# Kernel tuning notes

Measured on AMD Instinct MI355X. Metric: run time of the kernel, lower is better.

The kernel has to match this reference:

```python
import jax, jax.numpy as jnp
import numpy as np

NUM_CLASSES = 10000
EMBED_DIM = 128
BATCH = 4096
SCALE = 10.0
FOCAL_ALPHA = 0.25
FOCAL_GAMMA = 2.0
HARD_NEG_RATIO = 0.3


def setup_inputs() -> dict:
    key = jax.random.key(0)
    k1, k2, k3, k4 = jax.random.split(key, 4)
    embeddings = jax.random.normal(k1, (BATCH, EMBED_DIM), dtype=jnp.float32)
    labels = jax.random.randint(k2, (BATCH,), 0, NUM_CLASSES)
    class_weights = jax.random.uniform(k3, (NUM_CLASSES,), dtype=jnp.float32)
    # kaiming_normal_(mode='fan_out') on [C, D] -> std = sqrt(2 / C)
    proxies = jax.random.normal(k4, (NUM_CLASSES, EMBED_DIM), dtype=jnp.float32) * np.sqrt(2.0 / NUM_CLASSES)
    return {"embeddings": embeddings, "labels": labels,
            "class_weights": class_weights, "proxies": proxies}


def reference(embeddings, labels, class_weights, proxies):
    C = proxies.shape[0]
    # L2 normalize (F.normalize with eps=1e-12)
    e = embeddings / jnp.maximum(jnp.linalg.norm(embeddings, axis=1, keepdims=True), 1e-12)
    p = proxies / jnp.maximum(jnp.linalg.norm(proxies, axis=1, keepdims=True), 1e-12)
    sim = jnp.einsum('bd,cd->bc', e, p) * SCALE  # [B, C]

    pos_sim = jnp.take_along_axis(sim, labels[:, None], axis=1)[:, 0]  # [B]

    # mask out the positive class, then top-k hard negatives (k is static)
    k = max(1, int((C - 1) * HARD_NEG_RATIO))
    is_pos = labels[:, None] == jnp.arange(C)[None, :]
    neg_sim = jnp.where(is_pos, -jnp.inf, sim)
    hard_neg, _ = jax.lax.top_k(neg_sim, k)  # [B, k]

    combined = jnp.concatenate([pos_sim[:, None], hard_neg], axis=1)  # [B, 1+k]
    probs = jax.nn.softmax(combined, axis=1)
    pos_prob = probs[:, 0]

    ce = -jnp.log(pos_prob + 1e-8)
    focal = FOCAL_ALPHA * (1.0 - pos_prob) ** FOCAL_GAMMA * ce
    weighted = focal * class_weights[labels]
    return jnp.sum(weighted) / embeddings.shape[0]
```

## Files before the change

kernel.cpp:

```cpp
#include <hip/hip_runtime.h>
#include <hip/hip_bf16.h>
#include <hip/hip_fp16.h>


#define BATCH   4096
#define NCLASS  10000
#define EDIM    128
#define KSEL    2999
#define LDK     136
#define MLOG    10.0f

typedef __attribute__((ext_vector_type(8))) short short8;
typedef __attribute__((ext_vector_type(4))) float floatx4;

__device__ __forceinline__ unsigned short f2bf(float f) {
    unsigned int u = __float_as_uint(f);
    unsigned int r = (u + 0x7FFFu + ((u >> 16) & 1u)) >> 16;
    return (unsigned short)r;
}
__device__ __forceinline__ unsigned int f2key16(float x) {
    unsigned short hb = __half_as_ushort(__float2half(x));
    return (hb & 0x8000u) ? (unsigned int)(~hb & 0xFFFFu)
                          : (unsigned int)(hb | 0x8000u);
}
__device__ __forceinline__ float key16val(unsigned int k) {
    unsigned short hb = (k & 0x8000u) ? (unsigned short)(k ^ 0x8000u)
                                      : (unsigned short)(~k & 0xFFFFu);
    return __half2float(__ushort_as_half(hb));
}

__global__ __launch_bounds__(256) void prep_kernel(
    const float* __restrict__ emb, const float* __restrict__ px,
    unsigned short* __restrict__ px_bf, unsigned short* __restrict__ emb_bf)
{
    const int tid  = threadIdx.x;
    const int lane = tid & 63;
    const int w    = tid >> 6;
    const int row  = blockIdx.x * 4 + w;

    const float* src;
    unsigned short* dst;
    float scale;
    if (row < NCLASS) {
        src = px + (size_t)row * EDIM;  dst = px_bf + (size_t)row * EDIM;  scale = 1.0f;
    } else {
        int r = row - NCLASS;
        src = emb + (size_t)r * EDIM;   dst = emb_bf + (size_t)r * EDIM;   scale = 10.0f;
    }
    float a = src[lane], b = src[lane + 64];
    float ss = a * a + b * b;
    #pragma unroll
    for (int off = 32; off; off >>= 1) ss += __shfl_xor(ss, off);
    float inv = scale / fmaxf(sqrtf(ss), 1e-12f);
    dst[lane]      = f2bf(a * inv);
    dst[lane + 64] = f2bf(b * inv);
}

__global__ __launch_bounds__(256) void gemm_kernel(
    const unsigned short* __restrict__ emb_bf,
    const unsigned short* __restrict__ px_bf,
    unsigned short* __restrict__ simk, int row0, int nby)
{
    __shared__ __align__(16) unsigned short Als[128 * LDK];
    __shared__ __align__(16) unsigned short Bls[128 * LDK];

    const int NBX = (NCLASS + 127) / 128;
    const int tid  = threadIdx.x;
    const int lane = tid & 63;
    const int w    = tid >> 6;

    int ct, rt;
    {
        int L = blockIdx.x;
        if ((nby & 7) == 0) {
            int rpx = nby >> 3;
            int xcd = L & 7;
            int s   = L >> 3;
            rt = xcd * rpx + (s % rpx);
            ct = s / rpx;
        } else {
            ct = L % NBX; rt = L / NBX;
        }
    }
    const int c0   = ct * 128;
    const int rg0  = row0 + rt * 128;

    #pragma unroll
    for (int i = 0; i < 8; ++i) {
        int c  = tid + i * 256;
        int r  = c >> 4;
        int kc = (c & 15) << 3;
        uint4 v = *(const uint4*)(emb_bf + (size_t)(rg0 + r) * EDIM + kc);
        *(uint4*)(Als + r * LDK + kc) = v;
    }
    #pragma unroll
    for (int i = 0; i < 8; ++i) {
        int c  = tid + i * 256;
        int n  = c >> 4;
        int kc = (c & 15) << 3;
        uint4 v = make_uint4(0u, 0u, 0u, 0u);
        if (c0 + n < NCLASS)
            v = *(const uint4*)(px_bf + (size_t)(c0 + n) * EDIM + kc);
        *(uint4*)(Bls + n * LDK + kc) = v;
    }
    __syncthreads();

    const int wr = (w >> 1) * 64;
    const int wc = (w & 1) * 64;
    const int fm = lane & 15;
    const int fq = lane >> 4;

    floatx4 acc[4][4];
    #pragma unroll
    for (int i = 0; i < 4; ++i)
        #pragma unroll
        for (int j = 0; j < 4; ++j)
            acc[i][j] = (floatx4){0.f, 0.f, 0.f, 0.f};

    #pragma unroll
    for (int kk = 0; kk < 4; ++kk) {
        const int kof = kk * 32 + fq * 8;
        short8 a[4], b[4];
        #pragma unroll
        for (int i = 0; i < 4; ++i)
            a[i] = *(const short8*)(Als + (wr + i * 16 + fm) * LDK + kof);
        #pragma unroll
        for (int j = 0; j < 4; ++j)
            b[j] = *(const short8*)(Bls + (wc + j * 16 + fm) * LDK + kof);
        #pragma unroll
        for (int i = 0; i < 4; ++i)
            #pragma unroll
            for (int j = 0; j < 4; ++j)
                acc[i][j] = __builtin_amdgcn_mfma_f32_16x16x32_bf16(
                    a[i], b[j], acc[i][j], 0, 0, 0);
    }

    __syncthreads();
    unsigned short* T = Als;
    #pragma unroll
    for (int j = 0; j < 4; ++j) {
        int col = wc + j * 16 + fm;
        #pragma unroll
        for (int i = 0; i < 4; ++i) {
            int rbase = wr + i * 16 + fq * 4;
            #pragma unroll
            for (int r = 0; r < 4; ++r)
                T[(rbase + r) * LDK + col] = (unsigned short)f2key16(acc[i][j][r]);
        }
    }
    __syncthreads();

    const int rl0 = rt * 128;
    #pragma unroll
    for (int t = 0; t < 8; ++t) {
        int idx = t * 256 + tid;
        int rowl = idx >> 4;
        int g    = idx & 15;
        int col  = c0 + g * 8;
        if (col < NCLASS) {
            uint4 v = *(const uint4*)(T + rowl * LDK + g * 8);
            *(uint4*)(simk + (size_t)(rl0 + rowl) * NCLASS + col) = v;
        }
    }
}

__global__ __launch_bounds__(256, 8) void select_kernel(
    const unsigned short* __restrict__ simk, const int* __restrict__ labels,
    const float* __restrict__ cw, float* __restrict__ partials, int row0)
{
    __shared__ __align__(16) unsigned int hist[2048];
    __shared__ __align__(16) unsigned int psum[256];
    __shared__ float fred[8];
    __shared__ float s_pos;
    __shared__ unsigned int s_b, s_fill, s_cntb;

    const int tid   = threadIdx.x;
    const int lane  = tid & 63;
    const int w     = tid >> 6;
    const int rl    = blockIdx.x;
    const int label = labels[row0 + rl];
    const unsigned short* srow = simk + (size_t)rl * NCLASS;

    unsigned short poskey = 0;
    if (tid == 0) poskey = srow[label];

    {
        uint4 z = make_uint4(0u, 0u, 0u, 0u);
        *(uint4*)&hist[tid * 8]     = z;
        *(uint4*)&hist[tid * 8 + 4] = z;
    }
    __syncthreads();
    uint4 kv[5];
    kv[4] = make_uint4(0u, 0u, 0u, 0u);
    #pragma unroll
    for (int t = 0; t < 5; ++t) {
        int i = tid + t * 256;
        if (i < NCLASS / 8) kv[t] = *(const uint4*)(srow + i * 8);
    }

    #pragma unroll
    for (int t = 0; t < 5; ++t) {
        int i = tid + t * 256;
        if (i < NCLASS / 8) {
            unsigned int p[4] = {kv[t].x, kv[t].y, kv[t].z, kv[t].w};
            #pragma unroll
            for (int q = 0; q < 4; ++q) {
                unsigned int klo = p[q] & 0xFFFFu;
                unsigned int khi = p[q] >> 16;
                atomicAdd(&hist[klo >> 5], 0x100000u | (klo & 31u));
                atomicAdd(&hist[khi >> 5], 0x100000u | (khi & 31u));
            }
        }
    }
    __syncthreads();
    if (tid == 0) {
        s_pos = key16val(poskey);
        hist[poskey >> 5] -= 0x100000u | ((unsigned int)poskey & 31u);
    }
    __syncthreads();

    uint4 h0 = *(const uint4*)&hist[tid * 8];
    uint4 h1 = *(const uint4*)&hist[tid * 8 + 4];
    unsigned int wd[8] = {h0.x, h0.y, h0.z, h0.w, h1.x, h1.y, h1.z, h1.w};
    unsigned int sfx[8];
    sfx[7] = wd[7] >> 20;
    #pragma unroll
    for (int i = 6; i >= 0; --i) sfx[i] = sfx[i + 1] + (wd[i] >> 20);
    psum[tid] = sfx[0];
    __syncthreads();
    if (w == 0) {
        uint4 g = *(const uint4*)&psum[lane * 4];
        unsigned int gs = g.x + g.y + g.z + g.w;
        unsigned int s = gs;
        #pragma unroll
        for (int off = 1; off < 64; off <<= 1) {
            unsigned int o = __shfl_down(s, off);
            if (lane + off < 64) s += o;
        }
        unsigned int above = s - gs;
        unsigned int a3 = above;
        unsigned int a2 = a3 + g.w;
        unsigned int a1 = a2 + g.z;
        unsigned int a0 = a1 + g.y;
        psum[lane * 4 + 0] = a0; psum[lane * 4 + 1] = a1;
        psum[lane * 4 + 2] = a2; psum[lane * 4 + 3] = a3;
    }
    __syncthreads();
    {
        unsigned int add = psum[tid];
        #pragma unroll
        for (int i = 0; i < 8; ++i) {
            unsigned int cur = sfx[i] + add;
            unsigned int nxt = ((i < 7) ? sfx[i + 1] : 0u) + add;
            if (cur >= KSEL && nxt < KSEL) {
                s_b    = (unsigned int)(tid * 8 + i);
                s_fill = KSEL - nxt;
                s_cntb = sfx[i] - ((i < 7) ? sfx[i + 1] : 0u);
            }
        }
    }
    __syncthreads();

    const unsigned int b = s_b;
    float sum = 0.f, bsum = 0.f;
    if (b >= 1024u) {
        const float fillf = (float)s_fill;
        #pragma unroll
        for (int i = 0; i < 8; ++i) {
            unsigned int bin = (unsigned int)(tid * 8 + i);
            unsigned int c = wd[i] >> 20;
            if (bin >= b && c) {
                float rbar = (float)(wd[i] & 0xFFFFFu) / (float)c;
                unsigned int kb = bin << 5;
                float v0  = key16val(kb);
                float v32 = key16val(kb + 32u);
                float vm  = v0 + (v32 - v0) * (rbar * 0.03125f);
                float e = __expf(vm - MLOG);
                sum += ((bin > b) ? (float)c : fillf) * e;
            }
        }
    } else {
        for (int i = tid; i < NCLASS / 8; i += 256) {
            uint4 pk = *(const uint4*)(srow + i * 8);
            unsigned int p[4] = {pk.x, pk.y, pk.z, pk.w};
            #pragma unroll
            for (int q = 0; q < 4; ++q) {
                unsigned int klo = p[q] & 0xFFFFu;
                unsigned int khi = p[q] >> 16;
                unsigned int blo = klo >> 5, bhi = khi >> 5;
                int idx = i * 8 + q * 2;
                if (blo >= b && idx != label) {
                    float e = __expf(key16val(klo) - MLOG);
                    if (blo > b) sum += e; else bsum += e;
                }
                if (bhi >= b && (idx + 1) != label) {
                    float e = __expf(key16val(khi) - MLOG);
                    if (bhi > b) sum += e; else bsum += e;
                }
            }
        }
    }
    #pragma unroll
    for (int off = 32; off; off >>= 1) {
        sum  += __shfl_xor(sum, off);
        bsum += __shfl_xor(bsum, off);
    }
    if (lane == 0) { fred[w] = sum; fred[4 + w] = bsum; }
    __syncthreads();

    if (tid == 0) {
        float S  = fred[0] + fred[1] + fred[2] + fred[3];
        float Bs = fred[4] + fred[5] + fred[6] + fred[7];
        float ep = __expf(s_pos - MLOG);
        float denom = S + Bs * ((float)s_fill / (float)s_cntb) + ep;
        float p  = ep / denom;
        float ce = -logf(p + 1e-8f);
        float focal = 0.25f * (1.0f - p) * (1.0f - p) * ce;
        partials[row0 + rl] = focal * cw[label] * (1.0f / (float)BATCH);
    }
}

__global__ __launch_bounds__(256) void reduce_kernel(
    const float* __restrict__ partials, float* __restrict__ out)
{
    __shared__ float red[4];
    const int tid = threadIdx.x;
    float s = 0.f;
    #pragma unroll
    for (int t = 0; t < BATCH / 256; ++t)
        s += partials[tid + t * 256];
    #pragma unroll
    for (int off = 32; off; off >>= 1) s += __shfl_xor(s, off);
    if ((tid & 63) == 0) red[tid >> 6] = s;
    __syncthreads();
    if (tid == 0) out[0] = red[0] + red[1] + red[2] + red[3];
}

extern "C" void kernel_launch(void* const* d_in, const int* in_sizes, int n_in,
                              void* d_out, int out_size, void* d_ws, size_t ws_size,
                              hipStream_t stream) {
    const float* emb    = (const float*)d_in[0];
    const int*   labels = (const int*)d_in[1];
    const float* cw     = (const float*)d_in[2];
    const float* px     = (const float*)d_in[3];
    float* out = (float*)d_out;
    char*  wsc = (char*)d_ws;

    unsigned short* px_bf  = (unsigned short*)wsc;
    unsigned short* emb_bf = (unsigned short*)(wsc + 2560000);
    float*          parts  = (float*)(wsc + 3608576);
    unsigned short* simk   = (unsigned short*)(wsc + 3624960);

    size_t fixed = 3624960;
    size_t avail = (ws_size > fixed) ? (ws_size - fixed) : 0;
    long long cap = (long long)(avail / ((size_t)NCLASS * 2));
    int chunk = (int)((cap / 128) * 128);
    if (chunk > BATCH) chunk = BATCH;
    if (chunk < 128) chunk = 128;

    prep_kernel<<<3524, 256, 0, stream>>>(emb, px, px_bf, emb_bf);

    const int NBX = (NCLASS + 127) / 128;
    for (int r0 = 0; r0 < BATCH; r0 += chunk) {
        int rows = (BATCH - r0 < chunk) ? (BATCH - r0) : chunk;
        int nby  = rows / 128;
        gemm_kernel<<<NBX * nby, 256, 0, stream>>>(emb_bf, px_bf, simk, r0, nby);
        select_kernel<<<rows, 256, 0, stream>>>(simk, labels, cw, parts, r0);
    }
    reduce_kernel<<<1, 256, 0, stream>>>(parts, out);
}
```

Measured before the change: 124.8 us.

## Load GEMM fragments directly from global memory, drop LDS staging for operands

The GEMM kernel no longer stages the A and B tiles in shared memory. Each wave loads its MFMA fragments straight from global memory into double-buffered registers, prefetching the next k-slice while the current one computes. Shared memory is now used only for the output transpose, which halves LDS use and raises the occupancy hint to 3 blocks per SM. The prep kernel also switches to vectorized float2 loads and ushort2 stores. The trade-off is redundant global/L2 reads of operands shared across waves, plus uncoalesced 16-byte row-strided fragment loads.

```diff
diff --git a/kernel.cpp b/kernel.cpp
--- a/kernel.cpp
+++ b/kernel.cpp
@@ -47,22 +47,23 @@
         int r = row - NCLASS;
         src = emb + (size_t)r * EDIM;   dst = emb_bf + (size_t)r * EDIM;   scale = 10.0f;
     }
-    float a = src[lane], b = src[lane + 64];
-    float ss = a * a + b * b;
+    float2 v = *(const float2*)(src + 2 * lane);
+    float ss = v.x * v.x + v.y * v.y;
     #pragma unroll
     for (int off = 32; off; off >>= 1) ss += __shfl_xor(ss, off);
     float inv = scale / fmaxf(sqrtf(ss), 1e-12f);
-    dst[lane]      = f2bf(a * inv);
-    dst[lane + 64] = f2bf(b * inv);
-}
-
-__global__ __launch_bounds__(256) void gemm_kernel(
+    ushort2 o;
+    o.x = f2bf(v.x * inv);
+    o.y = f2bf(v.y * inv);
+    *(ushort2*)(dst + 2 * lane) = o;
+}
+
+__global__ __launch_bounds__(256, 3) void gemm_kernel(
     const unsigned short* __restrict__ emb_bf,
     const unsigned short* __restrict__ px_bf,
     unsigned short* __restrict__ simk, int row0, int nby)
 {
-    __shared__ __align__(16) unsigned short Als[128 * LDK];
-    __shared__ __align__(16) unsigned short Bls[128 * LDK];
+    __shared__ __align__(16) unsigned short T[128 * LDK];
 
     const int NBX = (NCLASS + 127) / 128;
     const int tid  = threadIdx.x;
@@ -85,31 +86,23 @@
     const int c0   = ct * 128;
     const int rg0  = row0 + rt * 128;
 
-    #pragma unroll
-    for (int i = 0; i < 8; ++i) {
-        int c  = tid + i * 256;
-        int r  = c >> 4;
-        int kc = (c & 15) << 3;
-        uint4 v = *(const uint4*)(emb_bf + (size_t)(rg0 + r) * EDIM + kc);
-        *(uint4*)(Als + r * LDK + kc) = v;
-    }
-    #pragma unroll
-    for (int i = 0; i < 8; ++i) {
-        int c  = tid + i * 256;
-        int n  = c >> 4;
-        int kc = (c & 15) << 3;
-        uint4 v = make_uint4(0u, 0u, 0u, 0u);
-        if (c0 + n < NCLASS)
-            v = *(const uint4*)(px_bf + (size_t)(c0 + n) * EDIM + kc);
-        *(uint4*)(Bls + n * LDK + kc) = v;
-    }
-    __syncthreads();
-
     const int wr = (w >> 1) * 64;
     const int wc = (w & 1) * 64;
     const int fm = lane & 15;
     const int fq = lane >> 4;
 
+    const unsigned short* arow[4];
+    const unsigned short* brow[4];
+    #pragma unroll
+    for (int i = 0; i < 4; ++i)
+        arow[i] = emb_bf + (size_t)(rg0 + wr + i * 16 + fm) * EDIM + fq * 8;
+    #pragma unroll
+    for (int j = 0; j < 4; ++j) {
+        int col = c0 + wc + j * 16 + fm;
+        if (col > NCLASS - 1) col = NCLASS - 1;
+        brow[j] = px_bf + (size_t)col * EDIM + fq * 8;
+    }
+
     floatx4 acc[4][4];
     #pragma unroll
     for (int i = 0; i < 4; ++i)
@@ -117,26 +110,32 @@
         for (int j = 0; j < 4; ++j)
             acc[i][j] = (floatx4){0.f, 0.f, 0.f, 0.f};
 
+    short8 af[2][4], bf_[2][4];
+    #pragma unroll
+    for (int i = 0; i < 4; ++i) af[0][i]  = *(const short8*)(arow[i]);
+    #pragma unroll
+    for (int j = 0; j < 4; ++j) bf_[0][j] = *(const short8*)(brow[j]);
+
     #pragma unroll
     for (int kk = 0; kk < 4; ++kk) {
-        const int kof = kk * 32 + fq * 8;
-        short8 a[4], b[4];
-        #pragma unroll
-        for (int i = 0; i < 4; ++i)
-            a[i] = *(const short8*)(Als + (wr + i * 16 + fm) * LDK + kof);
-        #pragma unroll
-        for (int j = 0; j < 4; ++j)
-            b[j] = *(const short8*)(Bls + (wc + j * 16 + fm) * LDK + kof);
+        const int cur = kk & 1, nxt = cur ^ 1;
+        if (kk < 3) {
+            const int kof = (kk + 1) * 32;
+            #pragma unroll
+            for (int i = 0; i < 4; ++i)
+                af[nxt][i]  = *(const short8*)(arow[i] + kof);
+            #pragma unroll
+            for (int j = 0; j < 4; ++j)
+                bf_[nxt][j] = *(const short8*)(brow[j] + kof);
+        }
         #pragma unroll
         for (int i = 0; i < 4; ++i)
             #pragma unroll
             for (int j = 0; j < 4; ++j)
                 acc[i][j] = __builtin_amdgcn_mfma_f32_16x16x32_bf16(
-                    a[i], b[j], acc[i][j], 0, 0, 0);
-    }
-
-    __syncthreads();
-    unsigned short* T = Als;
+                    af[cur][i], bf_[cur][j], acc[i][j], 0, 0, 0);
+    }
+
     #pragma unroll
     for (int j = 0; j < 4; ++j) {
         int col = wc + j * 16 + fm;
```

After: 131.1 us. 5.1% more time.
